# Kernel optimization log

Measured on AMD Instinct MI355X. Metric: run time of the kernel, lower is better.

Reference implementation:

```python
import jax, jax.numpy as jnp
import numpy as np
import math

EMBED_DIM = 1024
NUM_HEADS = 16
HEAD_DIM = EMBED_DIM // NUM_HEADS
ROPE_BASE = 10000.0


def _rope_cache(seq_len, dim, dtype=jnp.float32):
    inv_freq = 1.0 / (ROPE_BASE ** (jnp.arange(0, dim, 2, dtype=jnp.float32) / dim))
    t = jnp.arange(seq_len, dtype=jnp.float32)
    freqs = t[:, None] * inv_freq[None, :]          # [S, D/2]
    emb = jnp.concatenate([freqs, freqs], axis=-1)  # [S, D]
    return jnp.cos(emb).astype(dtype), jnp.sin(emb).astype(dtype)


def _rotate_half(x):
    x1, x2 = jnp.split(x, 2, axis=-1)
    return jnp.concatenate([-x2, x1], axis=-1)


def setup_inputs() -> dict:
    key = jax.random.key(0)
    ks = jax.random.split(key, 12)
    B, S, E = 2, 2048, EMBED_DIM
    s = 1.0 / math.sqrt(E)
    inp = {
        "query": jax.random.normal(ks[0], (B, S, E), jnp.float32),
        "key": jax.random.normal(ks[1], (B, S, E), jnp.float32),
        "value": jax.random.normal(ks[2], (B, S, E), jnp.float32),
        "Wq": jax.random.normal(ks[3], (E, E), jnp.float32) * s,
        "bq": jnp.zeros((E,), jnp.float32),
        "Wk": jax.random.normal(ks[4], (E, E), jnp.float32) * s,
        "bk": jnp.zeros((E,), jnp.float32),
        "Wv": jax.random.normal(ks[5], (E, E), jnp.float32) * s,
        "bv": jnp.zeros((E,), jnp.float32),
        "Wo": jax.random.normal(ks[6], (E, E), jnp.float32) * s,
        "bo": jnp.zeros((E,), jnp.float32),
    }
    return inp


def reference(query, key, value, Wq, bq, Wk, bk, Wv, bv, Wo, bo):
    B, S, E = query.shape
    H, D = NUM_HEADS, HEAD_DIM

    def proj(x, W, b):  # torch Linear: x @ W.T + b -> [B,H,S,D]
        return (x @ W.T + b).reshape(B, -1, H, D).transpose(0, 2, 1, 3)

    q = proj(query, Wq, bq)
    k = proj(key, Wk, bk)
    v = proj(value, Wv, bv)

    cos, sin = _rope_cache(S, D, q.dtype)  # [S, D]
    cos = cos[None, None]                  # [1,1,S,D]
    sin = sin[None, None]
    q = q * cos + _rotate_half(q) * sin
    k = k * cos + _rotate_half(k) * sin

    scale = 1.0 / math.sqrt(D)
    scores = jnp.einsum("bhsd,bhtd->bhst", q, k) * scale  # [B,H,S,S]
    causal = jnp.triu(jnp.ones((S, S), bool), k=1)
    scores = jnp.where(causal[None, None], -jnp.inf, scores)
    attn = jax.nn.softmax(scores, axis=-1)
    out = jnp.einsum("bhst,bhtd->bhsd", attn, v)           # [B,H,S,D]
    out = out.transpose(0, 2, 1, 3).reshape(B, S, E)
    return out @ Wo.T + bo
```

## Files before the change

### kernel.cpp

```cpp
#include <hip/hip_runtime.h>
#include <math.h>

typedef unsigned short u16;
typedef __attribute__((ext_vector_type(4))) float f32x4;
typedef __attribute__((ext_vector_type(8))) short bf16x8;

#define SEQ   2048
#define EMB   1024
#define NH    16
#define HD    64
#define MROWS 4096

__device__ __forceinline__ u16 f2b(float f) {
    unsigned u = __float_as_uint(f);
    u += 0x7fff + ((u >> 16) & 1);
    return (u16)(u >> 16);
}
__device__ __forceinline__ unsigned pack_bf16x2(float a, float b) {
    unsigned ua = __float_as_uint(a) + 0x8000u;
    unsigned ub = __float_as_uint(b) + 0x8000u;
    return __builtin_amdgcn_perm(ub, ua, 0x07060302u);
}
__device__ __forceinline__ void gld16(const u16* g, const u16* l) {
    __builtin_amdgcn_global_load_lds((const __attribute__((address_space(1))) void*)g,
                                     (__attribute__((address_space(3))) void*)l, 16, 0, 0);
}

struct F2BArgs { const float* s[7]; u16* d[7]; };

__global__ void k_f2b(F2BArgs a) {
    int id = blockIdx.x;
    const float* src; u16* dst; int base;
    if (id < 6144) {
        int z = id >> 11;
        src = a.s[z]; dst = a.d[z];
        base = (id & 2047) << 8;
    } else {
        int r = id - 6144;
        int z = 3 + (r >> 9);
        src = a.s[z]; dst = a.d[z];
        base = (r & 511) << 8;
    }
    int i = base + threadIdx.x;
    const float4* s4 = (const float4*)src;
    float4 x = s4[i * 2], y = s4[i * 2 + 1];
    union { u16 u[8]; uint4 v; } o;
    o.u[0] = f2b(x.x); o.u[1] = f2b(x.y); o.u[2] = f2b(x.z); o.u[3] = f2b(x.w);
    o.u[4] = f2b(y.x); o.u[5] = f2b(y.y); o.u[6] = f2b(y.z); o.u[7] = f2b(y.w);
    ((uint4*)dst)[i] = o.v;
}

struct GemmArgs {
    const u16* A; const u16* Bw; const float* bias; u16* Cb;
};

__global__ __launch_bounds__(256) void k_gemm_qkv(GemmArgs g0, GemmArgs g1, GemmArgs g2) {
    __shared__ u16 sbuf[2][8192];

    int id = blockIdx.x;
    int x = id / 96;
    int rem = id % 96;
    int z = rem >> 5;
    int y = rem & 31;
    GemmArgs g = (z == 0) ? g0 : (z == 1 ? g1 : g2);

    int tid = threadIdx.x;
    int wave = tid >> 6, lane = tid & 63, quad = lane >> 4, l16 = lane & 15;
    int wm = wave >> 1, wn = wave & 1;
    int m0 = y * 128, n0 = x * 128;
    const int K = EMB;

    auto stage = [&](int k0, u16* buf) {
#pragma unroll
        for (int pp = 0; pp < 4; pp++) {
            int slot = pp * 256 + tid;
            int p = slot & 3;
            const u16* gsrc;
            if (pp < 2) {
                int row = slot >> 2;
                int c = p ^ (row & 3);
                gsrc = g.A + (size_t)(m0 + row) * K + k0 + c * 8;
            } else {
                int row = (slot >> 2) - 128;
                int c = p ^ (row & 3);
                gsrc = g.Bw + (size_t)(n0 + row) * K + k0 + c * 8;
            }
            gld16(gsrc, buf + slot * 8);
        }
    };

    f32x4 acc[4][4];
#pragma unroll
    for (int i = 0; i < 4; i++)
#pragma unroll
        for (int j = 0; j < 4; j++) acc[i][j] = (f32x4){0.f, 0.f, 0.f, 0.f};

    int nk = K >> 5;
    stage(0, sbuf[0]);
    for (int ks = 0; ks < nk; ks++) {
        __syncthreads();
        if (ks + 1 < nk) stage((ks + 1) << 5, sbuf[(ks + 1) & 1]);
        const u16* Ab = sbuf[ks & 1];
        const u16* Bb = Ab + 4096;
        bf16x8 af[4], bfr[4];
#pragma unroll
        for (int i = 0; i < 4; i++) {
            int row = wm * 64 + i * 16 + l16;
            af[i] = *(const bf16x8*)&Ab[row * 32 + (quad ^ (row & 3)) * 8];
        }
#pragma unroll
        for (int j = 0; j < 4; j++) {
            int row = wn * 64 + j * 16 + l16;
            bfr[j] = *(const bf16x8*)&Bb[row * 32 + (quad ^ (row & 3)) * 8];
        }
#pragma unroll
        for (int i = 0; i < 4; i++)
#pragma unroll
            for (int j = 0; j < 4; j++)
                acc[i][j] = __builtin_amdgcn_mfma_f32_16x16x32_bf16(af[i], bfr[j], acc[i][j], 0, 0, 0);
    }

    if (z < 2) {
        float qscale = (z == 0) ? 0.18033688011112042f : 1.0f;
#pragma unroll
        for (int j = 0; j < 2; j++) {
            int col1 = n0 + wn * 64 + j * 16 + l16;
            int dd1 = col1 & 63;
            int h = col1 >> 6;
            float inv = __expf(-(float)dd1 * 0.28782313662425575f);
            float b1 = g.bias[col1], b2 = g.bias[col1 + 32];
#pragma unroll
            for (int i = 0; i < 4; i++)
#pragma unroll
                for (int r = 0; r < 4; r++) {
                    int row = m0 + wm * 64 + i * 16 + quad * 4 + r;
                    int b = row >> 11, s = row & (SEQ - 1);
                    float sn, cs;
                    __sincosf((float)s * inv, &sn, &cs);
                    float x1 = acc[i][j][r] + b1;
                    float x2 = acc[i][j + 2][r] + b2;
                    size_t base = ((size_t)(b * NH + h) * SEQ + s) << 6;
                    g.Cb[base + dd1]      = f2b((x1 * cs - x2 * sn) * qscale);
                    g.Cb[base + dd1 + 32] = f2b((x2 * cs + x1 * sn) * qscale);
                }
        }
    } else {
        __syncthreads();
        u16* tr = &sbuf[0][0] + wave * 4096;
        int h = (n0 >> 6) + wn;
        int b = m0 >> 11;
        int s0 = (m0 & (SEQ - 1)) + wm * 64;
#pragma unroll
        for (int j = 0; j < 4; j++) {
            float bv = g.bias[n0 + wn * 64 + j * 16 + l16];
#pragma unroll
            for (int i = 0; i < 4; i++) {
                uint2 pk;
                pk.x = pack_bf16x2(acc[i][j][0] + bv, acc[i][j][1] + bv);
                pk.y = pack_bf16x2(acc[i][j][2] + bv, acc[i][j][3] + bv);
                int row = j * 16 + l16;
                int c4 = i * 4 + quad;
                *(uint2*)&tr[row * 64 + ((c4 ^ (row & 14)) << 2)] = pk;
            }
        }
        u16* dst = g.Cb + (((size_t)(b * NH + h) * HD) * SEQ) + s0;
#pragma unroll
        for (int ps = 0; ps < 8; ps++) {
            int d = ps * 8 + (lane >> 3);
            int c4 = (lane & 7) * 2;
            uint4 v = *(const uint4*)&tr[d * 64 + ((c4 ^ (d & 14)) << 2)];
            *(uint4*)&dst[(size_t)d * SEQ + c4 * 4] = v;
        }
    }
}

__global__ __launch_bounds__(256) void k_gemm_o(const u16* __restrict__ A,
                                                const u16* __restrict__ Bw,
                                                const float* __restrict__ bias,
                                                float* __restrict__ C) {
    __shared__ u16 sb[2][6144];
    int tid = threadIdx.x;
    int w = tid >> 6, lane = tid & 63, quad = lane >> 4, l16 = lane & 15;
    int y = blockIdx.x & 63, x = blockIdx.x >> 6;
    int m0 = y * 64, n0 = x * 128;
    const int K = EMB;

    auto stage = [&](int k0, u16* buf) {
#pragma unroll
        for (int pp = 0; pp < 3; pp++) {
            int slot = pp * 256 + tid;
            if (slot < 256) {
                int row = slot >> 2, p = slot & 3;
                int c = p ^ (row & 3);
                gld16(A + (size_t)(m0 + row) * K + k0 + c * 8, buf + slot * 8);
            } else {
                int s2 = slot - 256;
                int row = s2 >> 2, p = s2 & 3;
                int c = p ^ (row & 3);
                gld16(Bw + (size_t)(n0 + row) * K + k0 + c * 8, buf + 2048 + s2 * 8);
            }
        }
    };

    f32x4 acc[4][2];
#pragma unroll
    for (int i = 0; i < 4; i++)
#pragma unroll
        for (int j = 0; j < 2; j++) acc[i][j] = (f32x4){0.f, 0.f, 0.f, 0.f};

    int nk = K >> 5;
    stage(0, sb[0]);
    for (int ks = 0; ks < nk; ks++) {
        __syncthreads();
        if (ks + 1 < nk) stage((ks + 1) << 5, sb[(ks + 1) & 1]);
        const u16* Ab = sb[ks & 1];
        const u16* Bb = Ab + 2048;
        bf16x8 af[4], bf[2];
#pragma unroll
        for (int i = 0; i < 4; i++) {
            int row = i * 16 + l16;
            af[i] = *(const bf16x8*)&Ab[row * 32 + (quad ^ (row & 3)) * 8];
        }
#pragma unroll
        for (int j = 0; j < 2; j++) {
            int row = w * 32 + j * 16 + l16;
            bf[j] = *(const bf16x8*)&Bb[row * 32 + (quad ^ (row & 3)) * 8];
        }
#pragma unroll
        for (int i = 0; i < 4; i++)
#pragma unroll
            for (int j = 0; j < 2; j++)
                acc[i][j] = __builtin_amdgcn_mfma_f32_16x16x32_bf16(af[i], bf[j], acc[i][j], 0, 0, 0);
    }

#pragma unroll
    for (int i = 0; i < 4; i++)
#pragma unroll
        for (int r = 0; r < 4; r++) {
            int row = m0 + i * 16 + quad * 4 + r;
#pragma unroll
            for (int j = 0; j < 2; j++) {
                int col = n0 + w * 32 + j * 16 + l16;
                C[(size_t)row * EMB + col] = acc[i][j][r] + bias[col];
            }
        }
}

__global__ __launch_bounds__(256, 2) void k_attn(const u16* __restrict__ Q,
                                                 const u16* __restrict__ K,
                                                 const u16* __restrict__ Vt,
                                                 u16* __restrict__ O) {
    __shared__ u16 sbuf[2][8192];
    __shared__ u16 Pl[4][2048];
    int tid = threadIdx.x;
    int w = tid >> 6, lane = tid & 63, quad = lane >> 4, l16 = lane & 15;
    int bh = blockIdx.x & 31;
    int qt = 15 - (blockIdx.x >> 5);
    int q0w = qt * 128 + w * 32;

    const u16* Qb = Q + (size_t)bh * SEQ * HD;
    const u16* Kb = K + (size_t)bh * SEQ * HD;
    const u16* Vb = Vt + (size_t)bh * HD * SEQ;
    u16* pl = Pl[w];

    auto stage = [&](int t0, u16* buf) {
#pragma unroll
        for (int pp = 0; pp < 4; pp++) {
            int slot = pp * 256 + tid;
            int r = (slot >> 3) & 63;
            int p = slot & 7;
            int c = p ^ (r & 7);
            const u16* gsrc = (pp < 2) ? Kb + (size_t)(t0 + r) * HD + c * 8
                                       : Vb + (size_t)r * SEQ + t0 + c * 8;
            gld16(gsrc, buf + slot * 8);
        }
    };

    bf16x8 bq[2][2];
#pragma unroll
    for (int g = 0; g < 2; g++) {
        size_t base = (size_t)(q0w + g * 16 + l16) * HD + quad * 8;
        bq[g][0] = *(const bf16x8*)&Qb[base];
        bq[g][1] = *(const bf16x8*)&Qb[base + 32];
    }

    f32x4 o2[2][4];
#pragma unroll
    for (int g = 0; g < 2; g++)
#pragma unroll
        for (int jd = 0; jd < 4; jd++) o2[g][jd] = (f32x4){0.f, 0.f, 0.f, 0.f};
    float l_p[2] = {0.f, 0.f};

    int niter = 2 * qt + 2;
    stage(0, sbuf[0]);
    for (int it = 0; it < niter; ++it) {
        __syncthreads();
        if (it + 1 < niter) stage((it + 1) * 64, sbuf[(it + 1) & 1]);
        const u16* Kl = sbuf[it & 1];
        const u16* Vl = Kl + 4096;
        int t0 = it * 64;

        bf16x8 kf[4][2], vf[4][2];
#pragma unroll
        for (int mt = 0; mt < 4; mt++) {
            int row = mt * 16 + l16;
            kf[mt][0] = *(const bf16x8*)&Kl[row * 64 + (quad ^ (row & 7)) * 8];
            kf[mt][1] = *(const bf16x8*)&Kl[row * 64 + ((quad + 4) ^ (row & 7)) * 8];
            vf[mt][0] = *(const bf16x8*)&Vl[row * 64 + (quad ^ (row & 7)) * 8];
            vf[mt][1] = *(const bf16x8*)&Vl[row * 64 + ((quad + 4) ^ (row & 7)) * 8];
        }

#pragma unroll
        for (int g = 0; g < 2; g++) {
            int qmin = q0w + g * 16;
            if (t0 > qmin + 15) continue;

            f32x4 sc[4];
#pragma unroll
            for (int mt = 0; mt < 4; mt++) {
                sc[mt] = (f32x4){0.f, 0.f, 0.f, 0.f};
                sc[mt] = __builtin_amdgcn_mfma_f32_16x16x32_bf16(kf[mt][0], bq[g][0], sc[mt], 0, 0, 0);
                sc[mt] = __builtin_amdgcn_mfma_f32_16x16x32_bf16(kf[mt][1], bq[g][1], sc[mt], 0, 0, 0);
            }

            if (t0 + 63 > qmin) {
                int q = qmin + l16;
#pragma unroll
                for (int mt = 0; mt < 4; mt++)
#pragma unroll
                    for (int r = 0; r < 4; r++) {
                        int t = t0 + mt * 16 + quad * 4 + r;
                        if (t > q) sc[mt][r] = -INFINITY;
                    }
            }

            float rs = 0.f;
#pragma unroll
            for (int mt = 0; mt < 4; mt++)
#pragma unroll
                for (int r = 0; r < 4; r++) {
                    float p = __builtin_amdgcn_exp2f(sc[mt][r] - 64.f);
                    sc[mt][r] = p;
                    rs += p;
                }
            l_p[g] += rs;

            u16* plg = pl + g * 1024;
#pragma unroll
            for (int mt = 0; mt < 4; mt++) {
                uint2 pk;
                pk.x = pack_bf16x2(sc[mt][0], sc[mt][1]);
                pk.y = pack_bf16x2(sc[mt][2], sc[mt][3]);
                int chunk = 2 * mt + (quad >> 1);
                *(uint2*)&plg[l16 * 64 + (chunk ^ (l16 & 7)) * 8 + (quad & 1) * 4] = pk;
            }

            bf16x8 pb0 = *(const bf16x8*)&plg[l16 * 64 + (quad ^ (l16 & 7)) * 8];
            bf16x8 pb1 = *(const bf16x8*)&plg[l16 * 64 + ((quad + 4) ^ (l16 & 7)) * 8];

#pragma unroll
            for (int jd = 0; jd < 4; jd++) {
                o2[g][jd] = __builtin_amdgcn_mfma_f32_16x16x32_bf16(vf[jd][0], pb0, o2[g][jd], 0, 0, 0);
                o2[g][jd] = __builtin_amdgcn_mfma_f32_16x16x32_bf16(vf[jd][1], pb1, o2[g][jd], 0, 0, 0);
            }
        }
    }

    int b = bh >> 4, h = bh & (NH - 1);
#pragma unroll
    for (int g = 0; g < 2; g++) {
        float l = l_p[g];
        l += __shfl_xor(l, 16, 64);
        l += __shfl_xor(l, 32, 64);
        float inv = 1.f / l;
#pragma unroll
        for (int jd = 0; jd < 4; jd++) {
            uint2 pk;
            pk.x = pack_bf16x2(o2[g][jd][0] * inv, o2[g][jd][1] * inv);
            pk.y = pack_bf16x2(o2[g][jd][2] * inv, o2[g][jd][3] * inv);
            *(uint2*)&pl[l16 * 72 + jd * 16 + quad * 4] = pk;
        }
        int row = lane >> 2, dc = (lane & 3) * 16;
        uint4 d0 = *(const uint4*)&pl[row * 72 + dc];
        uint4 d1 = *(const uint4*)&pl[row * 72 + dc + 8];
        int q = q0w + g * 16 + row;
        size_t addr = (size_t)(b * SEQ + q) * EMB + h * HD + dc;
        *(uint4*)&O[addr] = d0;
        *(uint4*)&O[addr + 8] = d1;
    }
}

extern "C" void kernel_launch(void* const* d_in, const int* in_sizes, int n_in,
                              void* d_out, int out_size, void* d_ws, size_t ws_size,
                              hipStream_t stream) {
    const float* query = (const float*)d_in[0];
    const float* key_  = (const float*)d_in[1];
    const float* value = (const float*)d_in[2];
    const float* Wq = (const float*)d_in[3];
    const float* bq = (const float*)d_in[4];
    const float* Wk = (const float*)d_in[5];
    const float* bk = (const float*)d_in[6];
    const float* Wv = (const float*)d_in[7];
    const float* bv = (const float*)d_in[8];
    const float* Wo = (const float*)d_in[9];
    const float* bo = (const float*)d_in[10];
    float* out = (float*)d_out;

    char* ws = (char*)d_ws;
    const size_t MB = 1u << 20;
    u16* xq  = (u16*)(ws + 0 * MB);
    u16* xk  = (u16*)(ws + 8 * MB);
    u16* xv  = (u16*)(ws + 16 * MB);
    u16* wqb = (u16*)(ws + 24 * MB);
    u16* wkb = (u16*)(ws + 26 * MB);
    u16* wvb = (u16*)(ws + 28 * MB);
    u16* wob = (u16*)(ws + 30 * MB);
    u16* Qp  = (u16*)(ws + 32 * MB);
    u16* Kp  = (u16*)(ws + 40 * MB);
    u16* Vt  = (u16*)(ws + 48 * MB);
    u16* Ab  = xk;

    F2BArgs fa;
    fa.s[0] = query; fa.s[1] = key_; fa.s[2] = value;
    fa.s[3] = Wq; fa.s[4] = Wk; fa.s[5] = Wv; fa.s[6] = Wo;
    fa.d[0] = xq; fa.d[1] = xk; fa.d[2] = xv;
    fa.d[3] = wqb; fa.d[4] = wkb; fa.d[5] = wvb; fa.d[6] = wob;
    k_f2b<<<8192, 256, 0, stream>>>(fa);

    GemmArgs gq = { xq, wqb, bq, Qp };
    GemmArgs gk = { xk, wkb, bk, Kp };
    GemmArgs gv = { xv, wvb, bv, Vt };
    k_gemm_qkv<<<768, 256, 0, stream>>>(gq, gk, gv);

    k_attn<<<512, 256, 0, stream>>>(Qp, Kp, Vt, Ab);

    k_gemm_o<<<512, 256, 0, stream>>>(Ab, wob, bo, out);
}
```

Baseline: 217.1 us.

## Split attention KV loop across two wave groups with LDS reduction

The attention kernel now runs 512 threads per block: two groups of four waves share the same query rows, and each group processes alternating 64-key tiles. Each iteration stages two KV tiles, and at the end one group writes its partial O and row sums to LDS for the other to reduce and store. This doubles the parallelism along the KV dimension to raise occupancy and hide latency. The cost is larger LDS use, an extra reduction step and barrier, and imbalance on causal tiles where one group skips its tile.

```diff
diff --git a/kernel.cpp b/kernel.cpp
--- a/kernel.cpp
+++ b/kernel.cpp
@@ -246,17 +246,18 @@
         }
 }
 
-__global__ __launch_bounds__(256, 2) void k_attn(const u16* __restrict__ Q,
+__global__ __launch_bounds__(512, 4) void k_attn(const u16* __restrict__ Q,
                                                  const u16* __restrict__ K,
                                                  const u16* __restrict__ Vt,
                                                  u16* __restrict__ O) {
-    __shared__ u16 sbuf[2][8192];
-    __shared__ u16 Pl[4][2048];
+    __shared__ u16 kv[4][8192];
+    __shared__ u16 Pl[8][1024];
     int tid = threadIdx.x;
     int w = tid >> 6, lane = tid & 63, quad = lane >> 4, l16 = lane & 15;
+    int pair = w & 3, par = w >> 2;
     int bh = blockIdx.x & 31;
     int qt = 15 - (blockIdx.x >> 5);
-    int q0w = qt * 128 + w * 32;
+    int q0w = qt * 128 + pair * 32;
 
     const u16* Qb = Q + (size_t)bh * SEQ * HD;
     const u16* Kb = K + (size_t)bh * SEQ * HD;
@@ -265,12 +266,12 @@
 
     auto stage = [&](int t0, u16* buf) {
 #pragma unroll
-        for (int pp = 0; pp < 4; pp++) {
-            int slot = pp * 256 + tid;
+        for (int pp = 0; pp < 2; pp++) {
+            int slot = pp * 512 + tid;
             int r = (slot >> 3) & 63;
             int p = slot & 7;
             int c = p ^ (r & 7);
-            const u16* gsrc = (pp < 2) ? Kb + (size_t)(t0 + r) * HD + c * 8
+            const u16* gsrc = (pp < 1) ? Kb + (size_t)(t0 + r) * HD + c * 8
                                        : Vb + (size_t)r * SEQ + t0 + c * 8;
             gld16(gsrc, buf + slot * 8);
         }
@@ -291,14 +292,20 @@
         for (int jd = 0; jd < 4; jd++) o2[g][jd] = (f32x4){0.f, 0.f, 0.f, 0.f};
     float l_p[2] = {0.f, 0.f};
 
-    int niter = 2 * qt + 2;
-    stage(0, sbuf[0]);
-    for (int it = 0; it < niter; ++it) {
+    int nsup = qt + 1;
+    stage(0, kv[0]);
+    stage(64, kv[2]);
+    for (int k = 0; k < nsup; ++k) {
         __syncthreads();
-        if (it + 1 < niter) stage((it + 1) * 64, sbuf[(it + 1) & 1]);
-        const u16* Kl = sbuf[it & 1];
+        if (k + 1 < nsup) {
+            stage((k + 1) * 128,      kv[(k + 1) & 1]);
+            stage((k + 1) * 128 + 64, kv[2 + ((k + 1) & 1)]);
+        }
+        int t0 = k * 128 + par * 64;
+        if (t0 > q0w + 31) continue;
+
+        const u16* Kl = kv[par * 2 + (k & 1)];
         const u16* Vl = Kl + 4096;
-        int t0 = it * 64;
 
         bf16x8 kf[4][2], vf[4][2];
 #pragma unroll
@@ -345,18 +352,17 @@
                 }
             l_p[g] += rs;
 
-            u16* plg = pl + g * 1024;
 #pragma unroll
             for (int mt = 0; mt < 4; mt++) {
                 uint2 pk;
                 pk.x = pack_bf16x2(sc[mt][0], sc[mt][1]);
                 pk.y = pack_bf16x2(sc[mt][2], sc[mt][3]);
                 int chunk = 2 * mt + (quad >> 1);
-                *(uint2*)&plg[l16 * 64 + (chunk ^ (l16 & 7)) * 8 + (quad & 1) * 4] = pk;
-            }
-
-            bf16x8 pb0 = *(const bf16x8*)&plg[l16 * 64 + (quad ^ (l16 & 7)) * 8];
-            bf16x8 pb1 = *(const bf16x8*)&plg[l16 * 64 + ((quad + 4) ^ (l16 & 7)) * 8];
+                *(uint2*)&pl[l16 * 64 + (chunk ^ (l16 & 7)) * 8 + (quad & 1) * 4] = pk;
+            }
+
+            bf16x8 pb0 = *(const bf16x8*)&pl[l16 * 64 + (quad ^ (l16 & 7)) * 8];
+            bf16x8 pb1 = *(const bf16x8*)&pl[l16 * 64 + ((quad + 4) ^ (l16 & 7)) * 8];
 
 #pragma unroll
             for (int jd = 0; jd < 4; jd++) {
@@ -366,6 +372,28 @@
         }
     }
 
+    __syncthreads();
+    float* mp = (float*)&kv[0][0] + pair * 2176;
+    if (par) {
+#pragma unroll
+        for (int g = 0; g < 2; g++) {
+#pragma unroll
+            for (int jd = 0; jd < 4; jd++)
+                *(f32x4*)&mp[(g * 4 + jd) * 256 + lane * 4] = o2[g][jd];
+            mp[2048 + g * 64 + lane] = l_p[g];
+        }
+    }
+    __syncthreads();
+    if (par) return;
+#pragma unroll
+    for (int g = 0; g < 2; g++) {
+#pragma unroll
+        for (int jd = 0; jd < 4; jd++)
+            o2[g][jd] += *(const f32x4*)&mp[(g * 4 + jd) * 256 + lane * 4];
+        l_p[g] += mp[2048 + g * 64 + lane];
+    }
+
+    u16* ep = ((u16*)&kv[0][0]) + 18432 + pair * 1216;
     int b = bh >> 4, h = bh & (NH - 1);
 #pragma unroll
     for (int g = 0; g < 2; g++) {
@@ -378,11 +406,11 @@
             uint2 pk;
             pk.x = pack_bf16x2(o2[g][jd][0] * inv, o2[g][jd][1] * inv);
             pk.y = pack_bf16x2(o2[g][jd][2] * inv, o2[g][jd][3] * inv);
-            *(uint2*)&pl[l16 * 72 + jd * 16 + quad * 4] = pk;
+            *(uint2*)&ep[l16 * 72 + jd * 16 + quad * 4] = pk;
         }
         int row = lane >> 2, dc = (lane & 3) * 16;
-        uint4 d0 = *(const uint4*)&pl[row * 72 + dc];
-        uint4 d1 = *(const uint4*)&pl[row * 72 + dc + 8];
+        uint4 d0 = *(const uint4*)&ep[row * 72 + dc];
+        uint4 d1 = *(const uint4*)&ep[row * 72 + dc + 8];
         int q = q0w + g * 16 + row;
         size_t addr = (size_t)(b * SEQ + q) * EMB + h * HD + dc;
         *(uint4*)&O[addr] = d0;
@@ -432,7 +460,7 @@
     GemmArgs gv = { xv, wvb, bv, Vt };
     k_gemm_qkv<<<768, 256, 0, stream>>>(gq, gk, gv);
 
-    k_attn<<<512, 256, 0, stream>>>(Qp, Kp, Vt, Ab);
+    k_attn<<<512, 512, 0, stream>>>(Qp, Kp, Vt, Ab);
 
     k_gemm_o<<<512, 256, 0, stream>>>(Ab, wob, bo, out);
 }
```

Result: slower. 315.5 us (+45.3%).
